# Optimization experiments

Hardware: AMD Instinct MI355X
Metric: run time of the kernel (lower is better)

The kernel has to match this reference:

```python
import jax, jax.numpy as jnp
import numpy as np

NUM_HEADS = 8


def setup_inputs() -> dict:
    key = jax.random.key(0)
    ks = jax.random.split(key, 5)
    B, C, H, W = 2, 256, 64, 64
    # 0.02 scaling keeps logits in a sane range so softmax is not one-hot
    return {
        "x": jax.random.normal(ks[0], (B, C, H, W), dtype=jnp.float32),
        "w_qkv": jax.random.normal(ks[1], (3 * C, C), dtype=jnp.float32) * 0.02,
        "b_qkv": jax.random.normal(ks[2], (3 * C,), dtype=jnp.float32) * 0.02,
        "w_proj": jax.random.normal(ks[3], (C, C), dtype=jnp.float32) * 0.02,
        "b_proj": jax.random.normal(ks[4], (C,), dtype=jnp.float32) * 0.02,
    }


def reference(x, w_qkv, b_qkv, w_proj, b_proj):
    B, C, H, W = x.shape
    N = H * W
    h = NUM_HEADS
    d = C // h
    # 1x1 conv == per-pixel linear: (B,C,H,W) -> (B,3C,H,W)
    qkv = jnp.einsum('oc,bchw->bohw', w_qkv, x) + b_qkv[None, :, None, None]
    qkv = qkv.reshape(B, 3, h, d, N)
    # q,k,v: (B, h, N, d)
    q = jnp.swapaxes(qkv[:, 0], -2, -1)
    k = jnp.swapaxes(qkv[:, 1], -2, -1)
    v = jnp.swapaxes(qkv[:, 2], -2, -1)
    scale = d ** (-0.5)
    attn = jax.nn.softmax(jnp.einsum('bhnd,bhmd->bhnm', q, k) * scale, axis=-1)
    out = jnp.einsum('bhnm,bhmd->bhnd', attn, v)  # (B, h, N, d)
    # faithful to torch: transpose(1,2) -> (B,N,h,d), then row-major reshape to (B,C,H,W)
    out = jnp.swapaxes(out, 1, 2).reshape(B, C, H, W)
    out = jnp.einsum('oc,bchw->bohw', w_proj, out) + b_proj[None, :, None, None]
    return out
```

## Files before the change

### kernel.cpp

```cpp
#include <hip/hip_runtime.h>
#include <hip/hip_bf16.h>


typedef __bf16 bf16;
typedef __bf16 bf16x4 __attribute__((ext_vector_type(4)));
typedef __bf16 bf16x8 __attribute__((ext_vector_type(8)));
typedef float  f32x4  __attribute__((ext_vector_type(4)));

#if __has_builtin(__builtin_amdgcn_mfma_f32_16x16x16bf16_1k)
#define HAVE_MFMA16 1
typedef short s16x4 __attribute__((ext_vector_type(4)));
#endif

#if __has_builtin(__builtin_amdgcn_exp2f)
#define EXP2(x) __builtin_amdgcn_exp2f(x)
#else
#define EXP2(x) exp2f(x)
#endif

#define NS 4096
#define QSCALE (0.17677669529663687f * 1.4426950408889634f)

__global__ __launch_bounds__(256) void xpose_x(
    const float* __restrict__ x, bf16* __restrict__ xt)
{
  __shared__ bf16 T[64 * 72];
  const int n0 = blockIdx.x * 64, c0 = blockIdx.y * 64, b = blockIdx.z;
  const int t = threadIdx.x;
  {
    const int cl = t & 63;
    const int np = (t >> 6) * 16;
    const float* src = x + ((size_t)(b * 256 + c0 + cl)) * NS + n0 + np;
#pragma unroll
    for (int j = 0; j < 16; j += 4) {
      f32x4 v = *(const f32x4*)(src + j);
#pragma unroll
      for (int i = 0; i < 4; i++) T[(np + j + i) * 72 + cl] = (bf16)v[i];
    }
  }
  __syncthreads();
  {
    const int nl = t & 63, hc = (t >> 6) * 16;
    bf16x8 r0 = *(const bf16x8*)&T[nl * 72 + hc];
    bf16x8 r1 = *(const bf16x8*)&T[nl * 72 + hc + 8];
    bf16* dst = xt + ((size_t)(b * NS + n0 + nl)) * 256 + c0 + hc;
    *(bf16x8*)dst = r0;
    *(bf16x8*)(dst + 8) = r1;
  }
}

__global__ __launch_bounds__(256) void qkv_mfma(
    const bf16* __restrict__ xt, const float* __restrict__ w,
    const float* __restrict__ bias,
    bf16* __restrict__ qbuf, bf16* __restrict__ kbuf, bf16* __restrict__ vbuf)
{
  __shared__ bf16 As[64 * 264];
  __shared__ bf16 Bs[64 * 264];
  const int n0 = blockIdx.x * 64, o0 = blockIdx.y * 64, b = blockIdx.z;
  const int t = threadIdx.x;
  const int wv = t >> 6, L = t & 63, quad = L >> 4, lb = L & 15;

  {
    const int r = t & 63, cb = (t >> 6) * 64;
    const bf16* xr = xt + ((size_t)(b * NS + n0 + r)) * 256 + cb;
    const float* wr = w + (size_t)(o0 + r) * 256 + cb;
#pragma unroll
    for (int j = 0; j < 64; j += 8) {
      *(bf16x8*)&As[r * 264 + cb + j] = *(const bf16x8*)(xr + j);
      f32x4 w0 = *(const f32x4*)(wr + j), w1 = *(const f32x4*)(wr + j + 4);
      bf16x8 wb;
#pragma unroll
      for (int i = 0; i < 4; i++) { wb[i] = (bf16)w0[i]; wb[4 + i] = (bf16)w1[i]; }
      *(bf16x8*)&Bs[r * 264 + cb + j] = wb;
    }
  }
  __syncthreads();

  f32x4 acc[4] = {};
#pragma unroll
  for (int ks = 0; ks < 8; ks++) {
    const bf16x8 bfr = *(const bf16x8*)&Bs[(wv * 16 + lb) * 264 + ks * 32 + quad * 8];
#pragma unroll
    for (int a = 0; a < 4; a++) {
      const bf16x8 afr = *(const bf16x8*)&As[(a * 16 + lb) * 264 + ks * 32 + quad * 8];
      acc[a] = __builtin_amdgcn_mfma_f32_16x16x32_bf16(afr, bfr, acc[a], 0, 0, 0);
    }
  }

  const int comp = o0 >> 8;
  const int o = o0 + wv * 16 + lb;
  const float bv = bias[o];
  if (comp < 2) {
    bf16* dst = (comp == 0) ? qbuf : kbuf;
    const float sc = (comp == 0) ? QSCALE : 1.0f;
    const int hh = (o & 255) >> 5, dd = o & 31;
    const size_t base = ((size_t)b * 8 + hh) * NS;
#pragma unroll
    for (int a = 0; a < 4; a++)
#pragma unroll
      for (int r = 0; r < 4; r++) {
        const int n = n0 + a * 16 + quad * 4 + r;
        dst[(base + n) * 32 + dd] = (bf16)((acc[a][r] + bv) * sc);
      }
  } else {
    __syncthreads();
    bf16* Vt2 = As;
#pragma unroll
    for (int a = 0; a < 4; a++)
#pragma unroll
      for (int r = 0; r < 4; r++)
        Vt2[(wv * 16 + lb) * 72 + a * 16 + quad * 4 + r] = (bf16)(acc[a][r] + bv);
    __syncthreads();
    const int row = t & 63;
    const int o2 = o0 + row;
    const int hh2 = (o2 & 255) >> 5, dd2 = o2 & 31;
    const int hc = (t >> 6) * 16;
    bf16x8 v0 = *(const bf16x8*)&Vt2[row * 72 + hc];
    bf16x8 v1 = *(const bf16x8*)&Vt2[row * 72 + hc + 8];
    bf16* vd = vbuf + (((size_t)b * 8 + hh2) * 32 + dd2) * NS + n0 + hc;
    *(bf16x8*)vd = v0;
    *(bf16x8*)(vd + 8) = v1;
  }
}

__global__ __launch_bounds__(256) void attn_kernel(
    const bf16* __restrict__ qbuf, const bf16* __restrict__ kbuf,
    const bf16* __restrict__ vbuf, bf16* __restrict__ abuf)
{
  __shared__ bf16 Ks[2][64 * 40];
  __shared__ bf16 Vts[2][32 * 72];
#ifndef HAVE_MFMA16
  __shared__ bf16 Ps[4][16 * 72];
#endif

  const int qb = blockIdx.x;
  const int bh = blockIdx.y;
  const bf16* Q  = qbuf + (size_t)bh * NS * 32;
  const bf16* K  = kbuf + (size_t)bh * NS * 32;
  const bf16* Vt = vbuf + (size_t)bh * 32 * NS;

  const int t = threadIdx.x;
  const int wv = t >> 6, L = t & 63, quad = L >> 4, lb = L & 15;
  const int qrow = qb * 64 + wv * 16;

  const bf16x8 qfrag = *(const bf16x8*)(Q + (size_t)(qrow + lb) * 32 + quad * 8);

  const int ki = t >> 2, kj = (t & 3) * 8;
  const int vr = t >> 3, vc = (t & 7) * 8;
  const bf16* Kg = K + (size_t)ki * 32 + kj;
  const bf16* Vg = Vt + (size_t)vr * NS + vc;

  bf16x8 kreg = *(const bf16x8*)Kg;
  bf16x8 vreg = *(const bf16x8*)Vg;

  f32x4 oacc0 = {0.f, 0.f, 0.f, 0.f};
  f32x4 oacc1 = {0.f, 0.f, 0.f, 0.f};
  float l_i = 0.f;
  const f32x4 zero4 = {0.f, 0.f, 0.f, 0.f};

#pragma unroll 2
  for (int kt = 0; kt < 64; kt++) {
    const int buf = kt & 1;
    *(bf16x8*)&Ks[buf][ki * 40 + kj] = kreg;
    *(bf16x8*)&Vts[buf][vr * 72 + vc] = vreg;
    __syncthreads();
    if (kt < 63) {
      kreg = *(const bf16x8*)(Kg + (size_t)(kt + 1) * 64 * 32);
      vreg = *(const bf16x8*)(Vg + (size_t)(kt + 1) * 64);
    }

    f32x4 st[4];
#pragma unroll
    for (int bi = 0; bi < 4; bi++) {
      const bf16x8 kf = *(const bf16x8*)&Ks[buf][(bi * 16 + lb) * 40 + quad * 8];
      st[bi] = __builtin_amdgcn_mfma_f32_16x16x32_bf16(kf, qfrag, zero4, 0, 0, 0);
    }

    float ls = 0.f;
#pragma unroll
    for (int bi = 0; bi < 4; bi++)
#pragma unroll
      for (int r = 0; r < 4; r++) {
        const float p = EXP2(st[bi][r]);
        st[bi][r] = p;
        ls += p;
      }
    l_i += ls;

#ifdef HAVE_MFMA16
#pragma unroll
    for (int bi = 0; bi < 4; bi++) {
      bf16x4 pb;
#pragma unroll
      for (int r = 0; r < 4; r++) pb[r] = (bf16)st[bi][r];
      const s16x4 pf = __builtin_bit_cast(s16x4, pb);
      const s16x4 vf0 = __builtin_bit_cast(s16x4,
          *(const bf16x4*)&Vts[buf][lb * 72 + bi * 16 + quad * 4]);
      const s16x4 vf1 = __builtin_bit_cast(s16x4,
          *(const bf16x4*)&Vts[buf][(16 + lb) * 72 + bi * 16 + quad * 4]);
      oacc0 = __builtin_amdgcn_mfma_f32_16x16x16bf16_1k(pf, vf0, oacc0, 0, 0, 0);
      oacc1 = __builtin_amdgcn_mfma_f32_16x16x16bf16_1k(pf, vf1, oacc1, 0, 0, 0);
    }
#else
    bf16* P = &Ps[wv][0];
#pragma unroll
    for (int bi = 0; bi < 4; bi++) {
      bf16x4 pk;
#pragma unroll
      for (int r = 0; r < 4; r++) pk[r] = (bf16)st[bi][r];
      *(bf16x4*)&P[lb * 72 + bi * 16 + quad * 4] = pk;
    }
#pragma unroll
    for (int ch = 0; ch < 2; ch++) {
      const bf16x8 pf  = *(const bf16x8*)&P[lb * 72 + ch * 32 + quad * 8];
      const bf16x8 vf0 = *(const bf16x8*)&Vts[buf][lb * 72 + ch * 32 + quad * 8];
      const bf16x8 vf1 = *(const bf16x8*)&Vts[buf][(16 + lb) * 72 + ch * 32 + quad * 8];
      oacc0 = __builtin_amdgcn_mfma_f32_16x16x32_bf16(pf, vf0, oacc0, 0, 0, 0);
      oacc1 = __builtin_amdgcn_mfma_f32_16x16x32_bf16(pf, vf1, oacc1, 0, 0, 0);
    }
#endif
    __syncthreads();
  }

  float lf = l_i;
  lf += __shfl_xor(lf, 16);
  lf += __shfl_xor(lf, 32);
  const int b_ = bh >> 3;
  const int hh = bh & 7;
#pragma unroll
  for (int r = 0; r < 4; r++) {
    const float lr = __shfl(lf, (quad << 4) | (quad * 4 + r));
#if __has_builtin(__builtin_amdgcn_rcpf)
    const float inv = __builtin_amdgcn_rcpf(lr);
#else
    const float inv = 1.0f / lr;
#endif
    const int n = qrow + quad * 4 + r;
    bf16* dst = abuf + ((size_t)b_ * NS + n) * 256 + hh * 32;
    dst[lb]      = (bf16)(oacc0[r] * inv);
    dst[16 + lb] = (bf16)(oacc1[r] * inv);
  }
}

__global__ __launch_bounds__(256) void xpose_a(
    const bf16* __restrict__ abuf, bf16* __restrict__ pbuf)
{
  __shared__ bf16 T[64 * 72];
  const int c0 = blockIdx.x * 64, ch0 = blockIdx.y * 64;
  const int z = blockIdx.z, b = z >> 4, sHi = z & 15;
  const int t = threadIdx.x;
  {
    const int cl  = t & 63;
    const int chp = (t >> 6) * 16;
    const bf16* src = abuf + ((size_t)b * NS + (size_t)(c0 + cl) * 16 + sHi) * 256 + ch0 + chp;
    bf16x8 a0 = *(const bf16x8*)src;
    bf16x8 a1 = *(const bf16x8*)(src + 8);
#pragma unroll
    for (int j = 0; j < 8; j++) {
      T[(chp + j) * 72 + cl] = a0[j];
      T[(chp + 8 + j) * 72 + cl] = a1[j];
    }
  }
  __syncthreads();
  {
    const int chl = t & 63, hc = (t >> 6) * 16;
    bf16x8 r0 = *(const bf16x8*)&T[chl * 72 + hc];
    bf16x8 r1 = *(const bf16x8*)&T[chl * 72 + hc + 8];
    bf16* dst = pbuf + ((size_t)z * 256 + ch0 + chl) * 256 + c0 + hc;
    *(bf16x8*)dst = r0;
    *(bf16x8*)(dst + 8) = r1;
  }
}

__global__ __launch_bounds__(256) void proj_mfma(
    const bf16* __restrict__ pbuf, const float* __restrict__ w,
    const float* __restrict__ bias, float* __restrict__ out)
{
  __shared__ bf16 As[64 * 264];
  __shared__ bf16 Bs[64 * 264];
  const int ch0 = blockIdx.x * 64, o0 = blockIdx.y * 64;
  const int z = blockIdx.z, b = z >> 4, sHi = z & 15;
  const int t = threadIdx.x;
  const int wv = t >> 6, L = t & 63, quad = L >> 4, lb = L & 15;

  {
    const int r = t & 63, cb = (t >> 6) * 64;
    const float* wr = w + (size_t)(o0 + r) * 256 + cb;
    const bf16* pr = pbuf + ((size_t)z * 256 + ch0 + r) * 256 + cb;
#pragma unroll
    for (int j = 0; j < 64; j += 8) {
      f32x4 w0 = *(const f32x4*)(wr + j), w1 = *(const f32x4*)(wr + j + 4);
      bf16x8 wb;
#pragma unroll
      for (int i = 0; i < 4; i++) { wb[i] = (bf16)w0[i]; wb[4 + i] = (bf16)w1[i]; }
      *(bf16x8*)&As[r * 264 + cb + j] = wb;
      *(bf16x8*)&Bs[r * 264 + cb + j] = *(const bf16x8*)(pr + j);
    }
  }
  __syncthreads();

  f32x4 acc[4] = {};
#pragma unroll
  for (int ks = 0; ks < 8; ks++) {
    const bf16x8 bfr = *(const bf16x8*)&Bs[(wv * 16 + lb) * 264 + ks * 32 + quad * 8];
#pragma unroll
    for (int a = 0; a < 4; a++) {
      const bf16x8 afr = *(const bf16x8*)&As[(a * 16 + lb) * 264 + ks * 32 + quad * 8];
      acc[a] = __builtin_amdgcn_mfma_f32_16x16x32_bf16(afr, bfr, acc[a], 0, 0, 0);
    }
  }

  const int ch = ch0 + wv * 16 + lb;
#pragma unroll
  for (int a = 0; a < 4; a++)
#pragma unroll
    for (int r = 0; r < 4; r++) {
      const int o = o0 + a * 16 + quad * 4 + r;
      out[((size_t)b * 256 + o) * NS + sHi * 256 + ch] = acc[a][r] + bias[o];
    }
}

extern "C" void kernel_launch(void* const* d_in, const int* in_sizes, int n_in,
                              void* d_out, int out_size, void* d_ws, size_t ws_size,
                              hipStream_t stream) {
  const float* x      = (const float*)d_in[0];
  const float* w_qkv  = (const float*)d_in[1];
  const float* b_qkv  = (const float*)d_in[2];
  const float* w_proj = (const float*)d_in[3];
  const float* b_proj = (const float*)d_in[4];
  float* out = (float*)d_out;

  char* ws = (char*)d_ws;
  const size_t MB = 1024 * 1024;
  bf16* qbuf = (bf16*)(ws);
  bf16* kbuf = (bf16*)(ws + 4 * MB);
  bf16* vbuf = (bf16*)(ws + 8 * MB);
  bf16* abuf = (bf16*)(ws + 12 * MB);
  bf16* xt   = (bf16*)(ws + 16 * MB);
  bf16* pbuf = (bf16*)(ws + 20 * MB);

  xpose_x<<<dim3(64, 4, 2), 256, 0, stream>>>(x, xt);
  qkv_mfma<<<dim3(64, 12, 2), 256, 0, stream>>>(xt, w_qkv, b_qkv, qbuf, kbuf, vbuf);
  attn_kernel<<<dim3(64, 16), 256, 0, stream>>>(qbuf, kbuf, vbuf, abuf);
  xpose_a<<<dim3(4, 4, 32), 256, 0, stream>>>(abuf, pbuf);
  proj_mfma<<<dim3(4, 4, 32), 256, 0, stream>>>(pbuf, w_proj, b_proj, out);
}
```

Before: 176.2 us.

## Fuse transposes into QKV and projection GEMMs, compute softmax row sums via MFMA

Removes the two standalone transpose kernels. The QKV GEMM now reads fp32 x directly and transposes it into LDS as packed bf16 pairs. The projection GEMM gathers the attention output with the head-interleaving permutation straight into LDS. In attention, row sums are now accumulated by an extra MFMA against a ones vector instead of scalar adds and shuffles. The trailing per-iteration barrier is dropped in the MFMA16 path, and the V tile stride is padded to 80. This cuts launches and intermediate global round trips. The costs are repeated fp32 x reads across output blocks, scalar strided LDS stores in the projection gather, and one extra MFMA per tile.

After: 179.7 us. Within noise of the previous version (+2.0%).

```diff
diff --git a/kernel.cpp b/kernel.cpp
--- a/kernel.cpp
+++ b/kernel.cpp
@@ -6,10 +6,10 @@
 typedef __bf16 bf16x4 __attribute__((ext_vector_type(4)));
 typedef __bf16 bf16x8 __attribute__((ext_vector_type(8)));
 typedef float  f32x4  __attribute__((ext_vector_type(4)));
+typedef short  s16x4  __attribute__((ext_vector_type(4)));
 
 #if __has_builtin(__builtin_amdgcn_mfma_f32_16x16x16bf16_1k)
 #define HAVE_MFMA16 1
-typedef short s16x4 __attribute__((ext_vector_type(4)));
 #endif
 
 #if __has_builtin(__builtin_amdgcn_exp2f)
@@ -21,36 +21,14 @@
 #define NS 4096
 #define QSCALE (0.17677669529663687f * 1.4426950408889634f)
 
-__global__ __launch_bounds__(256) void xpose_x(
-    const float* __restrict__ x, bf16* __restrict__ xt)
-{
-  __shared__ bf16 T[64 * 72];
-  const int n0 = blockIdx.x * 64, c0 = blockIdx.y * 64, b = blockIdx.z;
-  const int t = threadIdx.x;
-  {
-    const int cl = t & 63;
-    const int np = (t >> 6) * 16;
-    const float* src = x + ((size_t)(b * 256 + c0 + cl)) * NS + n0 + np;
-#pragma unroll
-    for (int j = 0; j < 16; j += 4) {
-      f32x4 v = *(const f32x4*)(src + j);
-#pragma unroll
-      for (int i = 0; i < 4; i++) T[(np + j + i) * 72 + cl] = (bf16)v[i];
-    }
-  }
-  __syncthreads();
-  {
-    const int nl = t & 63, hc = (t >> 6) * 16;
-    bf16x8 r0 = *(const bf16x8*)&T[nl * 72 + hc];
-    bf16x8 r1 = *(const bf16x8*)&T[nl * 72 + hc + 8];
-    bf16* dst = xt + ((size_t)(b * NS + n0 + nl)) * 256 + c0 + hc;
-    *(bf16x8*)dst = r0;
-    *(bf16x8*)(dst + 8) = r1;
-  }
-}
-
-__global__ __launch_bounds__(256) void qkv_mfma(
-    const bf16* __restrict__ xt, const float* __restrict__ w,
+static __device__ inline unsigned pack2(float a, float b) {
+  union { bf16 h[2]; unsigned u; } v;
+  v.h[0] = (bf16)a; v.h[1] = (bf16)b;
+  return v.u;
+}
+
+__global__ __launch_bounds__(256) void qkv_fused(
+    const float* __restrict__ x, const float* __restrict__ w,
     const float* __restrict__ bias,
     bf16* __restrict__ qbuf, bf16* __restrict__ kbuf, bf16* __restrict__ vbuf)
 {
@@ -61,17 +39,35 @@
   const int wv = t >> 6, L = t & 63, quad = L >> 4, lb = L & 15;
 
   {
-    const int r = t & 63, cb = (t >> 6) * 64;
-    const bf16* xr = xt + ((size_t)(b * NS + n0 + r)) * 256 + cb;
-    const float* wr = w + (size_t)(o0 + r) * 256 + cb;
-#pragma unroll
-    for (int j = 0; j < 64; j += 8) {
-      *(bf16x8*)&As[r * 264 + cb + j] = *(const bf16x8*)(xr + j);
-      f32x4 w0 = *(const f32x4*)(wr + j), w1 = *(const f32x4*)(wr + j + 4);
-      bf16x8 wb;
-#pragma unroll
-      for (int i = 0; i < 4; i++) { wb[i] = (bf16)w0[i]; wb[4 + i] = (bf16)w1[i]; }
-      *(bf16x8*)&Bs[r * 264 + cb + j] = wb;
+    unsigned* A32 = (unsigned*)As;
+    const int nj = (t & 15) * 4;
+#pragma unroll
+    for (int p = 0; p < 8; p++) {
+      const int c = p * 32 + (t >> 4) * 2;
+      const float* xr = x + ((size_t)(b * 256 + c)) * NS + n0 + nj;
+      f32x4 va = *(const f32x4*)xr;
+      f32x4 vb = *(const f32x4*)(xr + NS);
+#pragma unroll
+      for (int i = 0; i < 4; i++)
+        A32[(nj + i) * 132 + (c >> 1)] = pack2(va[i], vb[i]);
+    }
+  }
+  {
+    const int cj = (t & 15) * 16;
+#pragma unroll
+    for (int p = 0; p < 4; p++) {
+      const int r = p * 16 + (t >> 4);
+      const float* wr = w + (size_t)(o0 + r) * 256 + cj;
+      f32x4 w0 = *(const f32x4*)wr,       w1 = *(const f32x4*)(wr + 4);
+      f32x4 w2 = *(const f32x4*)(wr + 8), w3 = *(const f32x4*)(wr + 12);
+      bf16x8 lo, hi;
+#pragma unroll
+      for (int i = 0; i < 4; i++) {
+        lo[i] = (bf16)w0[i]; lo[4 + i] = (bf16)w1[i];
+        hi[i] = (bf16)w2[i]; hi[4 + i] = (bf16)w3[i];
+      }
+      *(bf16x8*)&Bs[r * 264 + cj] = lo;
+      *(bf16x8*)&Bs[r * 264 + cj + 8] = hi;
     }
   }
   __syncthreads();
@@ -128,7 +124,7 @@
     const bf16* __restrict__ vbuf, bf16* __restrict__ abuf)
 {
   __shared__ bf16 Ks[2][64 * 40];
-  __shared__ bf16 Vts[2][32 * 72];
+  __shared__ bf16 Vts[2][32 * 80];
 #ifndef HAVE_MFMA16
   __shared__ bf16 Ps[4][16 * 72];
 #endif
@@ -155,14 +151,19 @@
 
   f32x4 oacc0 = {0.f, 0.f, 0.f, 0.f};
   f32x4 oacc1 = {0.f, 0.f, 0.f, 0.f};
+  f32x4 oacc2 = {0.f, 0.f, 0.f, 0.f};
+  const f32x4 zero4 = {0.f, 0.f, 0.f, 0.f};
+#ifdef HAVE_MFMA16
+  const s16x4 ones = {(short)0x3F80, (short)0x3F80, (short)0x3F80, (short)0x3F80};
+#else
   float l_i = 0.f;
-  const f32x4 zero4 = {0.f, 0.f, 0.f, 0.f};
+#endif
 
 #pragma unroll 2
   for (int kt = 0; kt < 64; kt++) {
     const int buf = kt & 1;
     *(bf16x8*)&Ks[buf][ki * 40 + kj] = kreg;
-    *(bf16x8*)&Vts[buf][vr * 72 + vc] = vreg;
+    *(bf16x8*)&Vts[buf][vr * 80 + vc] = vreg;
     __syncthreads();
     if (kt < 63) {
       kreg = *(const bf16x8*)(Kg + (size_t)(kt + 1) * 64 * 32);
@@ -176,16 +177,10 @@
       st[bi] = __builtin_amdgcn_mfma_f32_16x16x32_bf16(kf, qfrag, zero4, 0, 0, 0);
     }
 
-    float ls = 0.f;
 #pragma unroll
     for (int bi = 0; bi < 4; bi++)
 #pragma unroll
-      for (int r = 0; r < 4; r++) {
-        const float p = EXP2(st[bi][r]);
-        st[bi][r] = p;
-        ls += p;
-      }
-    l_i += ls;
+      for (int r = 0; r < 4; r++) st[bi][r] = EXP2(st[bi][r]);
 
 #ifdef HAVE_MFMA16
 #pragma unroll
@@ -195,41 +190,56 @@
       for (int r = 0; r < 4; r++) pb[r] = (bf16)st[bi][r];
       const s16x4 pf = __builtin_bit_cast(s16x4, pb);
       const s16x4 vf0 = __builtin_bit_cast(s16x4,
-          *(const bf16x4*)&Vts[buf][lb * 72 + bi * 16 + quad * 4]);
+          *(const bf16x4*)&Vts[buf][lb * 80 + bi * 16 + quad * 4]);
       const s16x4 vf1 = __builtin_bit_cast(s16x4,
-          *(const bf16x4*)&Vts[buf][(16 + lb) * 72 + bi * 16 + quad * 4]);
+          *(const bf16x4*)&Vts[buf][(16 + lb) * 80 + bi * 16 + quad * 4]);
       oacc0 = __builtin_amdgcn_mfma_f32_16x16x16bf16_1k(pf, vf0, oacc0, 0, 0, 0);
       oacc1 = __builtin_amdgcn_mfma_f32_16x16x16bf16_1k(pf, vf1, oacc1, 0, 0, 0);
-    }
-#else
-    bf16* P = &Ps[wv][0];
-#pragma unroll
-    for (int bi = 0; bi < 4; bi++) {
-      bf16x4 pk;
-#pragma unroll
-      for (int r = 0; r < 4; r++) pk[r] = (bf16)st[bi][r];
-      *(bf16x4*)&P[lb * 72 + bi * 16 + quad * 4] = pk;
-    }
-#pragma unroll
-    for (int ch = 0; ch < 2; ch++) {
-      const bf16x8 pf  = *(const bf16x8*)&P[lb * 72 + ch * 32 + quad * 8];
-      const bf16x8 vf0 = *(const bf16x8*)&Vts[buf][lb * 72 + ch * 32 + quad * 8];
-      const bf16x8 vf1 = *(const bf16x8*)&Vts[buf][(16 + lb) * 72 + ch * 32 + quad * 8];
-      oacc0 = __builtin_amdgcn_mfma_f32_16x16x32_bf16(pf, vf0, oacc0, 0, 0, 0);
-      oacc1 = __builtin_amdgcn_mfma_f32_16x16x32_bf16(pf, vf1, oacc1, 0, 0, 0);
-    }
-#endif
-    __syncthreads();
-  }
-
+      oacc2 = __builtin_amdgcn_mfma_f32_16x16x16bf16_1k(pf, ones, oacc2, 0, 0, 0);
+    }
+#else
+    {
+      float ls = 0.f;
+#pragma unroll
+      for (int bi = 0; bi < 4; bi++)
+#pragma unroll
+        for (int r = 0; r < 4; r++) ls += st[bi][r];
+      l_i += ls;
+      bf16* P = &Ps[wv][0];
+#pragma unroll
+      for (int bi = 0; bi < 4; bi++) {
+        bf16x4 pk;
+#pragma unroll
+        for (int r = 0; r < 4; r++) pk[r] = (bf16)st[bi][r];
+        *(bf16x4*)&P[lb * 72 + bi * 16 + quad * 4] = pk;
+      }
+#pragma unroll
+      for (int ch = 0; ch < 2; ch++) {
+        const bf16x8 pf  = *(const bf16x8*)&P[lb * 72 + ch * 32 + quad * 8];
+        const bf16x8 vf0 = *(const bf16x8*)&Vts[buf][lb * 80 + ch * 32 + quad * 8];
+        const bf16x8 vf1 = *(const bf16x8*)&Vts[buf][(16 + lb) * 80 + ch * 32 + quad * 8];
+        oacc0 = __builtin_amdgcn_mfma_f32_16x16x32_bf16(pf, vf0, oacc0, 0, 0, 0);
+        oacc1 = __builtin_amdgcn_mfma_f32_16x16x32_bf16(pf, vf1, oacc1, 0, 0, 0);
+      }
+      __syncthreads();
+    }
+#endif
+  }
+
+  const int b_ = bh >> 3;
+  const int hh = bh & 7;
+#ifndef HAVE_MFMA16
   float lf = l_i;
   lf += __shfl_xor(lf, 16);
   lf += __shfl_xor(lf, 32);
-  const int b_ = bh >> 3;
-  const int hh = bh & 7;
+#endif
 #pragma unroll
   for (int r = 0; r < 4; r++) {
+#ifdef HAVE_MFMA16
+    const float lr = oacc2[r];
+#else
     const float lr = __shfl(lf, (quad << 4) | (quad * 4 + r));
+#endif
 #if __has_builtin(__builtin_amdgcn_rcpf)
     const float inv = __builtin_amdgcn_rcpf(lr);
 #else
@@ -242,38 +252,8 @@
   }
 }
 
-__global__ __launch_bounds__(256) void xpose_a(
-    const bf16* __restrict__ abuf, bf16* __restrict__ pbuf)
-{
-  __shared__ bf16 T[64 * 72];
-  const int c0 = blockIdx.x * 64, ch0 = blockIdx.y * 64;
-  const int z = blockIdx.z, b = z >> 4, sHi = z & 15;
-  const int t = threadIdx.x;
-  {
-    const int cl  = t & 63;
-    const int chp = (t >> 6) * 16;
-    const bf16* src = abuf + ((size_t)b * NS + (size_t)(c0 + cl) * 16 + sHi) * 256 + ch0 + chp;
-    bf16x8 a0 = *(const bf16x8*)src;
-    bf16x8 a1 = *(const bf16x8*)(src + 8);
-#pragma unroll
-    for (int j = 0; j < 8; j++) {
-      T[(chp + j) * 72 + cl] = a0[j];
-      T[(chp + 8 + j) * 72 + cl] = a1[j];
-    }
-  }
-  __syncthreads();
-  {
-    const int chl = t & 63, hc = (t >> 6) * 16;
-    bf16x8 r0 = *(const bf16x8*)&T[chl * 72 + hc];
-    bf16x8 r1 = *(const bf16x8*)&T[chl * 72 + hc + 8];
-    bf16* dst = pbuf + ((size_t)z * 256 + ch0 + chl) * 256 + c0 + hc;
-    *(bf16x8*)dst = r0;
-    *(bf16x8*)(dst + 8) = r1;
-  }
-}
-
-__global__ __launch_bounds__(256) void proj_mfma(
-    const bf16* __restrict__ pbuf, const float* __restrict__ w,
+__global__ __launch_bounds__(256) void proj_fused(
+    const bf16* __restrict__ abuf, const float* __restrict__ w,
     const float* __restrict__ bias, float* __restrict__ out)
 {
   __shared__ bf16 As[64 * 264];
@@ -284,17 +264,32 @@
   const int wv = t >> 6, L = t & 63, quad = L >> 4, lb = L & 15;
 
   {
-    const int r = t & 63, cb = (t >> 6) * 64;
-    const float* wr = w + (size_t)(o0 + r) * 256 + cb;
-    const bf16* pr = pbuf + ((size_t)z * 256 + ch0 + r) * 256 + cb;
-#pragma unroll
-    for (int j = 0; j < 64; j += 8) {
-      f32x4 w0 = *(const f32x4*)(wr + j), w1 = *(const f32x4*)(wr + j + 4);
-      bf16x8 wb;
-#pragma unroll
-      for (int i = 0; i < 4; i++) { wb[i] = (bf16)w0[i]; wb[4 + i] = (bf16)w1[i]; }
-      *(bf16x8*)&As[r * 264 + cb + j] = wb;
-      *(bf16x8*)&Bs[r * 264 + cb + j] = *(const bf16x8*)(pr + j);
+    const int cj = (t & 15) * 16;
+#pragma unroll
+    for (int p = 0; p < 4; p++) {
+      const int r = p * 16 + (t >> 4);
+      const float* wr = w + (size_t)(o0 + r) * 256 + cj;
+      f32x4 w0 = *(const f32x4*)wr,       w1 = *(const f32x4*)(wr + 4);
+      f32x4 w2 = *(const f32x4*)(wr + 8), w3 = *(const f32x4*)(wr + 12);
+      bf16x8 lo, hi;
+#pragma unroll
+      for (int i = 0; i < 4; i++) {
+        lo[i] = (bf16)w0[i]; lo[4 + i] = (bf16)w1[i];
+        hi[i] = (bf16)w2[i]; hi[4 + i] = (bf16)w3[i];
+      }
+      *(bf16x8*)&As[r * 264 + cj] = lo;
+      *(bf16x8*)&As[r * 264 + cj + 8] = hi;
+    }
+  }
+  {
+    const int chj = (t & 7) * 8;
+#pragma unroll
+    for (int p = 0; p < 8; p++) {
+      const int c = p * 32 + (t >> 3);
+      bf16x8 v = *(const bf16x8*)(abuf +
+          ((size_t)b * NS + (size_t)c * 16 + sHi) * 256 + ch0 + chj);
+#pragma unroll
+      for (int i = 0; i < 8; i++) Bs[(chj + i) * 264 + c] = v[i];
     }
   }
   __syncthreads();
@@ -336,12 +331,8 @@
   bf16* kbuf = (bf16*)(ws + 4 * MB);
   bf16* vbuf = (bf16*)(ws + 8 * MB);
   bf16* abuf = (bf16*)(ws + 12 * MB);
-  bf16* xt   = (bf16*)(ws + 16 * MB);
-  bf16* pbuf = (bf16*)(ws + 20 * MB);
-
-  xpose_x<<<dim3(64, 4, 2), 256, 0, stream>>>(x, xt);
-  qkv_mfma<<<dim3(64, 12, 2), 256, 0, stream>>>(xt, w_qkv, b_qkv, qbuf, kbuf, vbuf);
+
+  qkv_fused<<<dim3(64, 12, 2), 256, 0, stream>>>(x, w_qkv, b_qkv, qbuf, kbuf, vbuf);
   attn_kernel<<<dim3(64, 16), 256, 0, stream>>>(qbuf, kbuf, vbuf, abuf);
-  xpose_a<<<dim3(4, 4, 32), 256, 0, stream>>>(abuf, pbuf);
-  proj_mfma<<<dim3(4, 4, 32), 256, 0, stream>>>(pbuf, w_proj, b_proj, out);
-}
+  proj_fused<<<dim3(4, 4, 32), 256, 0, stream>>>(abuf, w_proj, b_proj, out);
+}
```
